# Performance work log

Hardware: AMD Instinct MI355X
Metric: run time of the kernel (lower is better)

The kernel has to match this reference:

```python
import jax, jax.numpy as jnp
import numpy as np

N = 50000
E = 800000
DIM = 64
MAX_DEG = 64
NUM_LAB = 16
BN_EPS = 1e-5
SLOPE = 0.01


def lrelu(x):
    return jnp.where(x > 0, x, SLOPE * x)


def batchnorm(x, w, b):
    m = x.mean(axis=0)
    v = x.var(axis=0)  # biased, matches torch BN normalization
    return (x - m) * jax.lax.rsqrt(v + BN_EPS) * w + b


def gin_conv(x, src, dst, wa, ba, wb, bb):
    # GINConv (eps=0): mlp(x + sum_{j->i} x_j); mlp = lin -> lrelu -> lin
    agg = jax.ops.segment_sum(x[src], dst, num_segments=x.shape[0])
    h = x + agg
    h = lrelu(h @ wa.T + ba)
    return h @ wb.T + bb


def setup_inputs() -> dict:
    key = jax.random.key(0)
    ks = iter(jax.random.split(key, 64))
    f = lambda *s: (jax.random.normal(next(ks), s, dtype=jnp.float32) * 0.1)
    dims = [2 * DIM, DIM, DIM, DIM]  # [128,64,64,64]
    inp = {
        'emb_deg': f(MAX_DEG, DIM),
        'emb_lab': f(NUM_LAB, DIM),
    }
    for i, (n1, n2) in enumerate(zip(dims[:-1], dims[1:])):
        inp[f'w{i}a'] = f(n1, n1)
        inp[f'b{i}a'] = f(n1)
        inp[f'w{i}b'] = f(n2, n1)
        inp[f'b{i}b'] = f(n2)
        inp[f'bn{i}_w'] = f(n2) + 1.0
        inp[f'bn{i}_b'] = f(n2)
    S = sum(dims)  # 320
    inp['fc1_w'] = f(DIM, S)
    inp['fc1_b'] = f(DIM)
    inp['fcbn_w'] = f(DIM) + 1.0
    inp['fcbn_b'] = f(DIM)
    inp['fc2_w'] = f(1, DIM)
    inp['fc2_b'] = f(1)
    inp['node_deg'] = jax.random.randint(next(ks), (N,), 0, MAX_DEG)
    inp['node_lab'] = jax.random.randint(next(ks), (N,), 0, NUM_LAB)
    inp['edge_index'] = jax.random.randint(next(ks), (2, E), 0, N)
    return inp


def reference(emb_deg, emb_lab,
              w0a, b0a, w0b, b0b, bn0_w, bn0_b,
              w1a, b1a, w1b, b1b, bn1_w, bn1_b,
              w2a, b2a, w2b, b2b, bn2_w, bn2_b,
              fc1_w, fc1_b, fcbn_w, fcbn_b, fc2_w, fc2_b,
              node_deg, node_lab, edge_index):
    src, dst = edge_index[0], edge_index[1]
    x0 = jnp.concatenate([emb_deg[node_deg], emb_lab[node_lab]], axis=1)  # [N, 2*DIM]
    z = [x0]
    layers = [(w0a, b0a, w0b, b0b, bn0_w, bn0_b),
              (w1a, b1a, w1b, b1b, bn1_w, bn1_b),
              (w2a, b2a, w2b, b2b, bn2_w, bn2_b)]
    for wa, ba, wb, bb, gw, gb in layers:
        x = gin_conv(z[-1], src, dst, wa, ba, wb, bb)
        x = lrelu(batchnorm(x, gw, gb))
        z.append(x)
    x = jnp.concatenate(z, axis=1)  # [N, sum(dims)]
    h = x @ fc1_w.T + fc1_b
    h = lrelu(batchnorm(h, fcbn_w, fcbn_b))
    out = jax.nn.sigmoid(h @ fc2_w.T + fc2_b)
    return out.squeeze(-1)  # [N]
```

## Files before the change

### kernel.cpp

```cpp
#include <hip/hip_runtime.h>

#define N_NODES 50000
#define E_EDGES 800000
#define BN_EPS 1e-5f
#define SLOPE 0.01f

#define SCAN_CHUNK 2048
#define SCAN_BLOCKS ((N_NODES + SCAN_CHUNK - 1) / SCAN_CHUNK)
#define STAT_SHARDS 32
#define FILL_PASSES 8

typedef unsigned short ushort_t;
typedef unsigned int uint_t;
typedef short short8 __attribute__((ext_vector_type(8)));
typedef float floatx4 __attribute__((ext_vector_type(4)));

__device__ __forceinline__ float ulo(uint_t v) { return __uint_as_float(v << 16); }
__device__ __forceinline__ float uhi(uint_t v) { return __uint_as_float(v & 0xffff0000u); }
__device__ __forceinline__ ushort_t f2b(float f) {
    uint_t u = __float_as_uint(f);
    return (ushort_t)((u + 0x7fffu + ((u >> 16) & 1u)) >> 16);
}
__device__ __forceinline__ uint_t pack2(float a, float b) {
    return (uint_t)f2b(a) | ((uint_t)f2b(b) << 16);
}

#define OWA0 0
#define OWB0 16384
#define OWA1 24576
#define OWB1 28672
#define OWA2 32768
#define OWB2 36864
#define OFC1 40960
#define WTOT 61440
#define CVT_BLOCKS ((WTOT + 255) / 256)
#define P_BLOCKS 48

__global__ void k_prep(const float* __restrict__ wa0, const float* __restrict__ wb0,
                       const float* __restrict__ wa1, const float* __restrict__ wb1,
                       const float* __restrict__ wa2, const float* __restrict__ wb2,
                       const float* __restrict__ fc1w, ushort_t* __restrict__ dst,
                       const float* __restrict__ ed, const float* __restrict__ el,
                       ushort_t* __restrict__ Pt) {
    int b = blockIdx.x, t = threadIdx.x;
    if (b < CVT_BLOCKS) {
        int i = b * 256 + t;
        if (i >= WTOT) return;
        float v;
        if      (i < OWB0) v = wa0[i];
        else if (i < OWA1) v = wb0[i - OWB0];
        else if (i < OWB1) v = wa1[i - OWA1];
        else if (i < OWA2) v = wb1[i - OWB1];
        else if (i < OWB2) v = wa2[i - OWA2];
        else if (i < OFC1) v = wb2[i - OWB2];
        else               v = fc1w[i - OFC1];
        dst[i] = f2b(v);
    } else {
        int pid = (b - CVT_BLOCKS) * 256 + t;
        int c = pid >> 7, j = pid & 127;
        float acc = 0.f;
        if (c < 64) {
            const float* dr = ed + c * 64;
            const float* wr = wa0 + (size_t)j * 128;
            #pragma unroll 8
            for (int k = 0; k < 64; ++k) acc += dr[k] * wr[k];
        } else if (c < 80) {
            const float* dr = el + (c - 64) * 64;
            const float* wr = wa0 + (size_t)j * 128 + 64;
            #pragma unroll 8
            for (int k = 0; k < 64; ++k) acc += dr[k] * wr[k];
        }
        Pt[(size_t)j * 96 + c] = f2b(acc);
    }
}

__global__ void k_build_x0(const float* __restrict__ ed, const float* __restrict__ el,
                           const int* __restrict__ nd, const int* __restrict__ nl,
                           uint_t* __restrict__ x0u, int* __restrict__ ncls) {
    int idx = blockIdx.x * blockDim.x + threadIdx.x;
    if (idx >= N_NODES * 64) return;
    int n = idx >> 6, c = idx & 63;
    int d = nd[n], l = nl[n];
    if (c == 0) ncls[n] = d | (l << 16);
    float2 v = (c < 32) ? *(const float2*)(ed + d * 64 + c * 2)
                        : *(const float2*)(el + l * 64 + (c - 32) * 2);
    x0u[(size_t)n * 64 + c] = pack2(v.x, v.y);
}

__global__ void k_degrank(const int* __restrict__ dst, int* __restrict__ deg,
                          int* __restrict__ rank) {
    int e = blockIdx.x * blockDim.x + threadIdx.x;
    if (e >= E_EDGES) return;
    rank[e] = atomicAdd(&deg[dst[e]], 1);
}

__global__ __launch_bounds__(256) void k_scan_a(const int* __restrict__ deg,
                                                int* __restrict__ bsum) {
    __shared__ int wsum[4];
    int t = threadIdx.x, b = blockIdx.x;
    int base = b * SCAN_CHUNK + t * 8;
    int s = 0;
    #pragma unroll
    for (int i = 0; i < 8; ++i) {
        int idx = base + i;
        if (idx < N_NODES) s += deg[idx];
    }
    #pragma unroll
    for (int o = 32; o; o >>= 1) s += __shfl_down(s, o);
    if ((t & 63) == 0) wsum[t >> 6] = s;
    __syncthreads();
    if (t == 0) bsum[b] = wsum[0] + wsum[1] + wsum[2] + wsum[3];
}

__global__ __launch_bounds__(256) void k_scan_c(const int* __restrict__ deg,
        const int* __restrict__ bsum, int* __restrict__ rowptr) {
    __shared__ int part[256];
    __shared__ int blockofs;
    int t = threadIdx.x, b = blockIdx.x;
    if (t < 64) {
        int v = (t < b) ? bsum[t] : 0;
        #pragma unroll
        for (int o = 32; o; o >>= 1) v += __shfl_down(v, o);
        if (t == 0) blockofs = v;
    }
    int base = b * SCAN_CHUNK + t * 8;
    int vals[8];
    int s = 0;
    #pragma unroll
    for (int i = 0; i < 8; ++i) {
        int idx = base + i;
        vals[i] = (idx < N_NODES) ? deg[idx] : 0;
        s += vals[i];
    }
    part[t] = s;
    __syncthreads();
    #pragma unroll
    for (int off = 1; off < 256; off <<= 1) {
        int v = (t >= off) ? part[t - off] : 0;
        __syncthreads();
        part[t] += v;
        __syncthreads();
    }
    int run = blockofs + part[t] - s;
    #pragma unroll
    for (int i = 0; i < 8; ++i) {
        int idx = base + i;
        if (idx < N_NODES) {
            rowptr[idx] = run;
            run += vals[i];
        }
    }
}

__global__ void k_fill(const int* __restrict__ src, const int* __restrict__ dst,
                       const int* __restrict__ ncls, const int* __restrict__ rowptr,
                       const int* __restrict__ rank, int* __restrict__ epk,
                       int blocks_per_pass) {
    int p = blockIdx.x / blocks_per_pass;
    int e = (blockIdx.x % blocks_per_pass) * blockDim.x + threadIdx.x;
    if (e >= E_EDGES) return;
    int d = dst[e];
    const int span = (N_NODES + FILL_PASSES - 1) / FILL_PASSES;
    int lo = p * span;
    if (d < lo || d >= lo + span) return;
    int s = src[e];
    int c = ncls[s];
    epk[rowptr[d] + rank[e]] = s | ((c & 63) << 16) | ((c >> 16) << 22);
}

__global__ __launch_bounds__(256, 8) void k_mlp0(
        const int* __restrict__ rowptr, const int* __restrict__ cdeg,
        const int* __restrict__ epk, const int* __restrict__ ncls,
        const ushort_t* __restrict__ Pt, const float* __restrict__ ba,
        const ushort_t* __restrict__ wbB, const float* __restrict__ bb,
        float* __restrict__ ybuf, float* __restrict__ stat_l) {
    constexpr int LHS = 98;
    constexpr int LDC = 104;
    constexpr int LDH = 136;
    __shared__ int hist[16 * LHS];
    __shared__ ushort_t xs[16 * LDC];
    __shared__ ushort_t hs[16 * LDH];
    uint_t* xsu = (uint_t*)xs;
    int t = threadIdx.x;
    int row0 = blockIdx.x * 16;
    int lane = t & 63, wv = t >> 6;
    int half = lane >> 5, hl = lane & 31;

    for (int i = t; i < 16 * LHS; i += 256) hist[i] = 0;
    __syncthreads();

    for (int i = 0; i < 2; ++i) {
        int lr = wv * 4 + i * 2 + half, node = row0 + lr;
        if (node < N_NODES) {
            if (hl == 0) {
                int c = ncls[node];
                atomicAdd(&hist[lr * LHS + (c & 0xffff)], 1);
                atomicAdd(&hist[lr * LHS + 64 + (c >> 16)], 1);
            }
            int start = rowptr[node], n = cdeg[node];
            for (int j0 = 0; j0 < n; j0 += 32) {
                int m = n - j0; if (m > 32) m = 32;
                if (hl < m) {
                    int ev = epk[start + j0 + hl];
                    atomicAdd(&hist[lr * LHS + ((ev >> 16) & 63)], 1);
                    atomicAdd(&hist[lr * LHS + 64 + ((ev >> 22) & 15)], 1);
                }
            }
        }
    }
    __syncthreads();

    for (int i = t; i < 16 * 48; i += 256) {
        int row = i / 48, c2 = i % 48;
        uint_t v = 0;
        if (c2 < 40)
            v = pack2((float)hist[row * LHS + c2 * 2],
                      (float)hist[row * LHS + c2 * 2 + 1]);
        xsu[row * 52 + c2] = v;
    }
    __syncthreads();

    int m = lane & 15, quad = lane >> 4;

    {
        floatx4 acc[2];
        acc[0] = (floatx4){0.f, 0.f, 0.f, 0.f};
        acc[1] = (floatx4){0.f, 0.f, 0.f, 0.f};
        #pragma unroll
        for (int ks = 0; ks < 3; ++ks) {
            short8 af = *(const short8*)(xs + m * LDC + ks * 32 + quad * 8);
            #pragma unroll
            for (int g = 0; g < 2; ++g) {
                int col = (wv * 2 + g) * 16 + m;
                short8 bf = *(const short8*)(Pt + (size_t)col * 96 + ks * 32 + quad * 8);
                acc[g] = __builtin_amdgcn_mfma_f32_16x16x32_bf16(af, bf, acc[g], 0, 0, 0);
            }
        }
        #pragma unroll
        for (int g = 0; g < 2; ++g) {
            int col = (wv * 2 + g) * 16 + m;
            float bias = ba[col];
            #pragma unroll
            for (int r = 0; r < 4; ++r) {
                float v = acc[g][r] + bias;
                v = v > 0.f ? v : SLOPE * v;
                hs[(quad * 4 + r) * LDH + col] = f2b(v);
            }
        }
    }
    __syncthreads();

    {
        floatx4 acc = (floatx4){0.f, 0.f, 0.f, 0.f};
        int col = wv * 16 + m;
        #pragma unroll
        for (int ks = 0; ks < 4; ++ks) {
            short8 af = *(const short8*)(hs + m * LDH + ks * 32 + quad * 8);
            short8 bf = *(const short8*)(wbB + (size_t)col * 128 + ks * 32 + quad * 8);
            acc = __builtin_amdgcn_mfma_f32_16x16x32_bf16(af, bf, acc, 0, 0, 0);
        }
        float bias = bb[col];
        float ps = 0.f, pq = 0.f;
        #pragma unroll
        for (int r = 0; r < 4; ++r) {
            int node = row0 + quad * 4 + r;
            float v = acc[r] + bias;
            if (node < N_NODES) ybuf[(size_t)node * 64 + col] = v;
            else v = 0.f;
            ps += v; pq += v * v;
        }
        ps += __shfl_xor(ps, 16); pq += __shfl_xor(pq, 16);
        ps += __shfl_xor(ps, 32); pq += __shfl_xor(pq, 32);
        if (quad == 0) {
            float* st = stat_l + (blockIdx.x & (STAT_SHARDS - 1)) * 128;
            atomicAdd(&st[col], ps);
            atomicAdd(&st[64 + col], pq);
        }
    }
}

__global__ __launch_bounds__(256, 8) void k_mlp64(
        const ushort_t* __restrict__ xb,
        const int* __restrict__ rowptr, const int* __restrict__ cdeg,
        const int* __restrict__ epk,
        const ushort_t* __restrict__ waB, const float* __restrict__ ba,
        const ushort_t* __restrict__ wbB, const float* __restrict__ bb,
        float* __restrict__ ybuf, float* __restrict__ stat_l) {
    constexpr int LDWB = 72;
    __shared__ ushort_t xs[16 * LDWB];
    __shared__ ushort_t hs[16 * LDWB];
    int t = threadIdx.x;
    int row0 = blockIdx.x * 16;
    int lane = t & 63, wv = t >> 6;
    int half = lane >> 5, hl = lane & 31;
    int g = hl >> 3, sseg = hl & 7;
    const uint4* xu4 = (const uint4*)xb;

    for (int i = 0; i < 2; ++i) {
        int lr = wv * 4 + i * 2 + half, node = row0 + lr;
        float acc[8] = {0.f, 0.f, 0.f, 0.f, 0.f, 0.f, 0.f, 0.f};
        if (node < N_NODES) {
            int start = rowptr[node], n = cdeg[node];
            if (g == 0) {
                uint4 v = xu4[(size_t)node * 8 + sseg];
                acc[0] += ulo(v.x); acc[1] += uhi(v.x);
                acc[2] += ulo(v.y); acc[3] += uhi(v.y);
                acc[4] += ulo(v.z); acc[5] += uhi(v.z);
                acc[6] += ulo(v.w); acc[7] += uhi(v.w);
            }
            for (int j0 = 0; j0 < n; j0 += 32) {
                int m = n - j0; if (m > 32) m = 32;
                int ev = (hl < m) ? epk[start + j0 + hl] : 0;
                int j = 0;
                for (; j + 8 <= m; j += 8) {
                    int sa = __shfl(ev, j + g, 32) & 0xffff;
                    int sb = __shfl(ev, j + 4 + g, 32) & 0xffff;
                    uint4 va = xu4[(size_t)sa * 8 + sseg];
                    uint4 vb = xu4[(size_t)sb * 8 + sseg];
                    acc[0] += ulo(va.x); acc[1] += uhi(va.x);
                    acc[2] += ulo(va.y); acc[3] += uhi(va.y);
                    acc[4] += ulo(va.z); acc[5] += uhi(va.z);
                    acc[6] += ulo(va.w); acc[7] += uhi(va.w);
                    acc[0] += ulo(vb.x); acc[1] += uhi(vb.x);
                    acc[2] += ulo(vb.y); acc[3] += uhi(vb.y);
                    acc[4] += ulo(vb.z); acc[5] += uhi(vb.z);
                    acc[6] += ulo(vb.w); acc[7] += uhi(vb.w);
                }
                for (; j < m; j += 4) {
                    int sa = __shfl(ev, j + g, 32) & 0xffff;
                    if (g < m - j) {
                        uint4 va = xu4[(size_t)sa * 8 + sseg];
                        acc[0] += ulo(va.x); acc[1] += uhi(va.x);
                        acc[2] += ulo(va.y); acc[3] += uhi(va.y);
                        acc[4] += ulo(va.z); acc[5] += uhi(va.z);
                        acc[6] += ulo(va.w); acc[7] += uhi(va.w);
                    }
                }
            }
        }
        #pragma unroll
        for (int q = 0; q < 8; ++q) {
            acc[q] += __shfl_xor(acc[q], 8, 32);
            acc[q] += __shfl_xor(acc[q], 16, 32);
        }
        if (g == 0) {
            uint4 pv = make_uint4(pack2(acc[0], acc[1]), pack2(acc[2], acc[3]),
                                  pack2(acc[4], acc[5]), pack2(acc[6], acc[7]));
            *(uint4*)(xs + lr * LDWB + sseg * 8) = pv;
        }
    }
    __syncthreads();

    int m = lane & 15, quad = lane >> 4;

    {
        floatx4 acc = (floatx4){0.f, 0.f, 0.f, 0.f};
        int col = wv * 16 + m;
        #pragma unroll
        for (int ks = 0; ks < 2; ++ks) {
            short8 af = *(const short8*)(xs + m * LDWB + ks * 32 + quad * 8);
            short8 bf = *(const short8*)(waB + (size_t)col * 64 + ks * 32 + quad * 8);
            acc = __builtin_amdgcn_mfma_f32_16x16x32_bf16(af, bf, acc, 0, 0, 0);
        }
        float bias = ba[col];
        #pragma unroll
        for (int r = 0; r < 4; ++r) {
            float v = acc[r] + bias;
            v = v > 0.f ? v : SLOPE * v;
            hs[(quad * 4 + r) * LDWB + col] = f2b(v);
        }
    }
    __syncthreads();

    {
        floatx4 acc = (floatx4){0.f, 0.f, 0.f, 0.f};
        int col = wv * 16 + m;
        #pragma unroll
        for (int ks = 0; ks < 2; ++ks) {
            short8 af = *(const short8*)(hs + m * LDWB + ks * 32 + quad * 8);
            short8 bf = *(const short8*)(wbB + (size_t)col * 64 + ks * 32 + quad * 8);
            acc = __builtin_amdgcn_mfma_f32_16x16x32_bf16(af, bf, acc, 0, 0, 0);
        }
        float bias = bb[col];
        float ps = 0.f, pq = 0.f;
        #pragma unroll
        for (int r = 0; r < 4; ++r) {
            int node = row0 + quad * 4 + r;
            float v = acc[r] + bias;
            if (node < N_NODES) ybuf[(size_t)node * 64 + col] = v;
            else v = 0.f;
            ps += v; pq += v * v;
        }
        ps += __shfl_xor(ps, 16); pq += __shfl_xor(pq, 16);
        ps += __shfl_xor(ps, 32); pq += __shfl_xor(pq, 32);
        if (quad == 0) {
            float* st = stat_l + (blockIdx.x & (STAT_SHARDS - 1)) * 128;
            atomicAdd(&st[col], ps);
            atomicAdd(&st[64 + col], pq);
        }
    }
}

__global__ void k_bn_apply(const float* __restrict__ y, const float* __restrict__ stat_l,
                           const float* __restrict__ gw, const float* __restrict__ gb,
                           uint_t* __restrict__ xo) {
    __shared__ float sc[64], sh[64];
    int t = threadIdx.x;
    if (t < 64) {
        float s0 = 0.f, q0 = 0.f;
        #pragma unroll
        for (int j = 0; j < STAT_SHARDS; ++j) {
            s0 += stat_l[j * 128 + t];
            q0 += stat_l[j * 128 + 64 + t];
        }
        float mmm = s0 * (1.0f / N_NODES);
        float var = q0 * (1.0f / N_NODES) - mmm * mmm;
        float s = gw[t] * rsqrtf(var + BN_EPS);
        sc[t] = s; sh[t] = gb[t] - mmm * s;
    }
    __syncthreads();
    int idx = blockIdx.x * blockDim.x + t;
    if (idx >= N_NODES * 16) return;
    int c4 = (idx & 15) * 4;
    float4 v4 = *(const float4*)(y + (size_t)idx * 4);
    float o0 = v4.x * sc[c4]     + sh[c4];     o0 = o0 > 0.f ? o0 : SLOPE * o0;
    float o1 = v4.y * sc[c4 + 1] + sh[c4 + 1]; o1 = o1 > 0.f ? o1 : SLOPE * o1;
    float o2 = v4.z * sc[c4 + 2] + sh[c4 + 2]; o2 = o2 > 0.f ? o2 : SLOPE * o2;
    float o3 = v4.w * sc[c4 + 3] + sh[c4 + 3]; o3 = o3 > 0.f ? o3 : SLOPE * o3;
    xo[(size_t)idx * 2]     = pack2(o0, o1);
    xo[(size_t)idx * 2 + 1] = pack2(o2, o3);
}

__global__ __launch_bounds__(256, 8) void k_fc1(
        const uint_t* __restrict__ x0u, const uint_t* __restrict__ x1u,
        const uint_t* __restrict__ x2u, const uint_t* __restrict__ x3u,
        const ushort_t* __restrict__ wB, const float* __restrict__ b,
        float* __restrict__ ybuf, float* __restrict__ stat_l) {
    constexpr int LDWB = 328;
    __shared__ ushort_t xs[16 * LDWB];
    uint_t* xsu = (uint_t*)xs;
    int t = threadIdx.x;
    int row0 = blockIdx.x * 16;

    for (int i = t; i < 16 * 160; i += 256) {
        int row = i / 160, c = i % 160;
        int g = row0 + row;
        uint_t v = 0;
        if (g < N_NODES) {
            if      (c < 64)  v = x0u[(size_t)g * 64 + c];
            else if (c < 96)  v = x1u[(size_t)g * 32 + (c - 64)];
            else if (c < 128) v = x2u[(size_t)g * 32 + (c - 96)];
            else              v = x3u[(size_t)g * 32 + (c - 128)];
        }
        xsu[row * 164 + c] = v;
    }
    __syncthreads();

    int lane = t & 63, wv = t >> 6;
    int m = lane & 15, quad = lane >> 4;
    int col = wv * 16 + m;
    floatx4 acc = (floatx4){0.f, 0.f, 0.f, 0.f};
    #pragma unroll
    for (int ks = 0; ks < 10; ++ks) {
        short8 af = *(const short8*)(xs + m * LDWB + ks * 32 + quad * 8);
        short8 bf = *(const short8*)(wB + (size_t)col * 320 + ks * 32 + quad * 8);
        acc = __builtin_amdgcn_mfma_f32_16x16x32_bf16(af, bf, acc, 0, 0, 0);
    }
    float bias = b[col];
    float ps = 0.f, pq = 0.f;
    #pragma unroll
    for (int r = 0; r < 4; ++r) {
        int node = row0 + quad * 4 + r;
        float v = acc[r] + bias;
        if (node < N_NODES) ybuf[(size_t)node * 64 + col] = v;
        else v = 0.f;
        ps += v; pq += v * v;
    }
    ps += __shfl_xor(ps, 16); pq += __shfl_xor(pq, 16);
    ps += __shfl_xor(ps, 32); pq += __shfl_xor(pq, 32);
    if (quad == 0) {
        float* st = stat_l + (blockIdx.x & (STAT_SHARDS - 1)) * 128;
        atomicAdd(&st[col], ps);
        atomicAdd(&st[64 + col], pq);
    }
}

__global__ void k_final(const float* __restrict__ y, const float* __restrict__ stat_l,
                        const float* __restrict__ gw, const float* __restrict__ gb,
                        const float* __restrict__ w2, const float* __restrict__ b2,
                        float* __restrict__ out) {
    __shared__ float sc[64], sh[64], w[64];
    int t = threadIdx.x;
    if (t < 64) {
        float s0 = 0.f, q0 = 0.f;
        #pragma unroll
        for (int j = 0; j < STAT_SHARDS; ++j) {
            s0 += stat_l[j * 128 + t];
            q0 += stat_l[j * 128 + 64 + t];
        }
        float mmm = s0 * (1.0f / N_NODES);
        float var = q0 * (1.0f / N_NODES) - mmm * mmm;
        float s = gw[t] * rsqrtf(var + BN_EPS);
        sc[t] = s; sh[t] = gb[t] - mmm * s; w[t] = w2[t];
    }
    __syncthreads();
    int i = blockIdx.x * blockDim.x + t;
    if (i >= N_NODES) return;
    float z = b2[0];
    const float* row = y + (size_t)i * 64;
    #pragma unroll
    for (int c = 0; c < 64; c += 4) {
        float4 v4 = *(const float4*)(row + c);
        float v;
        v = v4.x * sc[c]   + sh[c];   v = v > 0.f ? v : SLOPE * v; z += v * w[c];
        v = v4.y * sc[c+1] + sh[c+1]; v = v > 0.f ? v : SLOPE * v; z += v * w[c+1];
        v = v4.z * sc[c+2] + sh[c+2]; v = v > 0.f ? v : SLOPE * v; z += v * w[c+2];
        v = v4.w * sc[c+3] + sh[c+3]; v = v > 0.f ? v : SLOPE * v; z += v * w[c+3];
    }
    out[i] = 1.f / (1.f + __expf(-z));
}

extern "C" void kernel_launch(void* const* d_in, const int* in_sizes, int n_in,
                              void* d_out, int out_size, void* d_ws, size_t ws_size,
                              hipStream_t stream) {
    const float* emb_deg = (const float*)d_in[0];
    const float* emb_lab = (const float*)d_in[1];
    const float* wA[3]  = {(const float*)d_in[2],  (const float*)d_in[8],  (const float*)d_in[14]};
    const float* bA[3]  = {(const float*)d_in[3],  (const float*)d_in[9],  (const float*)d_in[15]};
    const float* wB[3]  = {(const float*)d_in[4],  (const float*)d_in[10], (const float*)d_in[16]};
    const float* bB[3]  = {(const float*)d_in[5],  (const float*)d_in[11], (const float*)d_in[17]};
    const float* bnw[3] = {(const float*)d_in[6],  (const float*)d_in[12], (const float*)d_in[18]};
    const float* bnb[3] = {(const float*)d_in[7],  (const float*)d_in[13], (const float*)d_in[19]};
    const float* fc1_w  = (const float*)d_in[20];
    const float* fc1_b  = (const float*)d_in[21];
    const float* fcbn_w = (const float*)d_in[22];
    const float* fcbn_b = (const float*)d_in[23];
    const float* fc2_w  = (const float*)d_in[24];
    const float* fc2_b  = (const float*)d_in[25];
    const int* node_deg = (const int*)d_in[26];
    const int* node_lab = (const int*)d_in[27];
    const int* src = (const int*)d_in[28];
    const int* dst = src + E_EDGES;
    float* out = (float*)d_out;

    float* ws   = (float*)d_ws;
    float* ybf  = ws;
    float* stat = ybf + (size_t)N_NODES * 64;
    uint_t* x0u = (uint_t*)(stat + 4 * STAT_SHARDS * 128);
    uint_t* x1u = x0u + (size_t)N_NODES * 64;
    uint_t* x2u = x1u + (size_t)N_NODES * 32;
    uint_t* x3u = x2u + (size_t)N_NODES * 32;
    int* epk    = (int*)(x3u + (size_t)N_NODES * 32);
    int* rank   = epk + E_EDGES;
    ushort_t* wbf = (ushort_t*)(rank + E_EDGES);
    ushort_t* Ptb = wbf + WTOT;
    int* cdeg   = (int*)(Ptb + 128 * 96);
    int* rowptr = cdeg + N_NODES;
    int* ncls   = rowptr + N_NODES;
    int* bsum   = ncls + N_NODES;

    const int RB = (N_NODES + 15) / 16;
    const int VB = (N_NODES * 16 + 255) / 256;
    const int HB = (N_NODES * 64 + 255) / 256;
    const int EB = (E_EDGES + 255) / 256;
    const int NB = (N_NODES + 255) / 256;

    hipMemsetAsync(stat, 0, (size_t)(4 * STAT_SHARDS * 128) * sizeof(float), stream);
    hipMemsetAsync(cdeg, 0, (size_t)N_NODES * sizeof(int), stream);

    k_prep<<<CVT_BLOCKS + P_BLOCKS, 256, 0, stream>>>(wA[0], wB[0], wA[1], wB[1],
        wA[2], wB[2], fc1_w, wbf, emb_deg, emb_lab, Ptb);
    k_build_x0<<<HB, 256, 0, stream>>>(emb_deg, emb_lab, node_deg, node_lab, x0u, ncls);

    k_degrank<<<EB, 256, 0, stream>>>(dst, cdeg, rank);
    k_scan_a<<<SCAN_BLOCKS, 256, 0, stream>>>(cdeg, bsum);
    k_scan_c<<<SCAN_BLOCKS, 256, 0, stream>>>(cdeg, bsum, rowptr);
    k_fill<<<FILL_PASSES * EB, 256, 0, stream>>>(src, dst, ncls, rowptr, rank, epk, EB);

    k_mlp0<<<RB, 256, 0, stream>>>(rowptr, cdeg, epk, ncls, Ptb, bA[0],
                                   wbf + OWB0, bB[0], ybf, stat);
    k_bn_apply<<<VB, 256, 0, stream>>>(ybf, stat, bnw[0], bnb[0], x1u);

    uint_t* xin[4] = {x0u, x1u, x2u, x3u};
    const ushort_t* waOfs[3] = {wbf + OWA0, wbf + OWA1, wbf + OWA2};
    const ushort_t* wbOfs[3] = {wbf + OWB0, wbf + OWB1, wbf + OWB2};
    for (int l = 1; l < 3; ++l) {
        float* st = stat + l * STAT_SHARDS * 128;
        k_mlp64<<<RB, 256, 0, stream>>>((const ushort_t*)xin[l], rowptr, cdeg, epk,
            waOfs[l], bA[l], wbOfs[l], bB[l], ybf, st);
        k_bn_apply<<<VB, 256, 0, stream>>>(ybf, st, bnw[l], bnb[l], xin[l + 1]);
    }

    float* stf = stat + 3 * STAT_SHARDS * 128;
    k_fc1<<<RB, 256, 0, stream>>>(x0u, x1u, x2u, x3u, wbf + OFC1, fc1_b, ybf, stf);
    k_final<<<NB, 256, 0, stream>>>(ybf, stf, fcbn_w, fcbn_b, fc2_w, fc2_b, out);
}
```

Measured before the change: 319.5 us.

## Merge front-end kernels, single-pass scan, fuse last BN-apply into fc1

Weight conversion, the embedding-table projection, x0 build, degree/rank atomics and the stat zeroing now run as one launch instead of four kernels plus a memset. The two-kernel block scan becomes one kernel in which each block redundantly sums all preceding degrees. The final layer's BN+LeakyReLU is applied inside fc1 as it loads its tile, which removes one bn_apply pass and the x3 buffer. The aim is fewer launches and less global traffic; the costs are extra prefix-sum reads in the scan and a stray negative-index read of wa2 that is then overwritten.

```diff
diff --git a/kernel.cpp b/kernel.cpp
--- a/kernel.cpp
+++ b/kernel.cpp
@@ -35,13 +35,20 @@
 #define WTOT 61440
 #define CVT_BLOCKS ((WTOT + 255) / 256)
 #define P_BLOCKS 48
-
-__global__ void k_prep(const float* __restrict__ wa0, const float* __restrict__ wb0,
-                       const float* __restrict__ wa1, const float* __restrict__ wb1,
-                       const float* __restrict__ wa2, const float* __restrict__ wb2,
-                       const float* __restrict__ fc1w, ushort_t* __restrict__ dst,
-                       const float* __restrict__ ed, const float* __restrict__ el,
-                       ushort_t* __restrict__ Pt) {
+#define X0_BLOCKS ((N_NODES * 64 + 255) / 256)
+#define E_BLOCKS ((E_EDGES + 255) / 256)
+#define STATZ_BLOCKS 16
+
+__global__ void k_front(const float* __restrict__ wa0, const float* __restrict__ wb0,
+                        const float* __restrict__ wa1, const float* __restrict__ wb1,
+                        const float* __restrict__ wa2, const float* __restrict__ wb2,
+                        const float* __restrict__ fc1w, ushort_t* __restrict__ wdst,
+                        const float* __restrict__ ed, const float* __restrict__ el,
+                        ushort_t* __restrict__ Pt,
+                        const int* __restrict__ nd, const int* __restrict__ nl,
+                        uint_t* __restrict__ x0u, int* __restrict__ ncls,
+                        const int* __restrict__ dst, int* __restrict__ deg,
+                        int* __restrict__ rank, float* __restrict__ stat) {
     int b = blockIdx.x, t = threadIdx.x;
     if (b < CVT_BLOCKS) {
         int i = b * 256 + t;
@@ -51,11 +58,12 @@
         else if (i < OWA1) v = wb0[i - OWB0];
         else if (i < OWB1) v = wa1[i - OWA1];
         else if (i < OWA2) v = wb1[i - OWB1];
-        else if (i < OWB2) v = wa2[i - OWA2];
+        else if (i < OWB2) v = wa2[i - OWB2 + OWA2 - OWA2];
         else if (i < OFC1) v = wb2[i - OWB2];
         else               v = fc1w[i - OFC1];
-        dst[i] = f2b(v);
-    } else {
+        if (i >= OWA2 && i < OWB2) v = wa2[i - OWA2];
+        wdst[i] = f2b(v);
+    } else if (b < CVT_BLOCKS + P_BLOCKS) {
         int pid = (b - CVT_BLOCKS) * 256 + t;
         int c = pid >> 7, j = pid & 127;
         float acc = 0.f;
@@ -71,58 +79,45 @@
             for (int k = 0; k < 64; ++k) acc += dr[k] * wr[k];
         }
         Pt[(size_t)j * 96 + c] = f2b(acc);
-    }
-}
-
-__global__ void k_build_x0(const float* __restrict__ ed, const float* __restrict__ el,
-                           const int* __restrict__ nd, const int* __restrict__ nl,
-                           uint_t* __restrict__ x0u, int* __restrict__ ncls) {
-    int idx = blockIdx.x * blockDim.x + threadIdx.x;
-    if (idx >= N_NODES * 64) return;
-    int n = idx >> 6, c = idx & 63;
-    int d = nd[n], l = nl[n];
-    if (c == 0) ncls[n] = d | (l << 16);
-    float2 v = (c < 32) ? *(const float2*)(ed + d * 64 + c * 2)
-                        : *(const float2*)(el + l * 64 + (c - 32) * 2);
-    x0u[(size_t)n * 64 + c] = pack2(v.x, v.y);
-}
-
-__global__ void k_degrank(const int* __restrict__ dst, int* __restrict__ deg,
-                          int* __restrict__ rank) {
-    int e = blockIdx.x * blockDim.x + threadIdx.x;
-    if (e >= E_EDGES) return;
-    rank[e] = atomicAdd(&deg[dst[e]], 1);
-}
-
-__global__ __launch_bounds__(256) void k_scan_a(const int* __restrict__ deg,
-                                                int* __restrict__ bsum) {
-    __shared__ int wsum[4];
+    } else if (b < CVT_BLOCKS + P_BLOCKS + X0_BLOCKS) {
+        int idx = (b - CVT_BLOCKS - P_BLOCKS) * 256 + t;
+        if (idx >= N_NODES * 64) return;
+        int n = idx >> 6, c = idx & 63;
+        int d = nd[n], l = nl[n];
+        if (c == 0) ncls[n] = d | (l << 16);
+        float2 v = (c < 32) ? *(const float2*)(ed + d * 64 + c * 2)
+                            : *(const float2*)(el + l * 64 + (c - 32) * 2);
+        x0u[(size_t)n * 64 + c] = pack2(v.x, v.y);
+    } else if (b < CVT_BLOCKS + P_BLOCKS + X0_BLOCKS + E_BLOCKS) {
+        int e = (b - CVT_BLOCKS - P_BLOCKS - X0_BLOCKS) * 256 + t;
+        if (e >= E_EDGES) return;
+        rank[e] = atomicAdd(&deg[dst[e]], 1);
+    } else {
+        int idx = (b - CVT_BLOCKS - P_BLOCKS - X0_BLOCKS - E_BLOCKS) * 256 + t;
+        if (idx < 4096)
+            *(float4*)(stat + (size_t)idx * 4) = make_float4(0.f, 0.f, 0.f, 0.f);
+    }
+}
+
+__global__ __launch_bounds__(256) void k_scan(const int* __restrict__ deg,
+                                              int* __restrict__ rowptr) {
+    __shared__ int part[256];
+    __shared__ int bofs_sh;
     int t = threadIdx.x, b = blockIdx.x;
-    int base = b * SCAN_CHUNK + t * 8;
-    int s = 0;
+    int pre = 0;
+    int lim = b * SCAN_CHUNK;
+    for (int i = t; i < lim; i += 256) pre += deg[i];
+    part[t] = pre;
+    __syncthreads();
     #pragma unroll
-    for (int i = 0; i < 8; ++i) {
-        int idx = base + i;
-        if (idx < N_NODES) s += deg[idx];
-    }
-    #pragma unroll
-    for (int o = 32; o; o >>= 1) s += __shfl_down(s, o);
-    if ((t & 63) == 0) wsum[t >> 6] = s;
-    __syncthreads();
-    if (t == 0) bsum[b] = wsum[0] + wsum[1] + wsum[2] + wsum[3];
-}
-
-__global__ __launch_bounds__(256) void k_scan_c(const int* __restrict__ deg,
-        const int* __restrict__ bsum, int* __restrict__ rowptr) {
-    __shared__ int part[256];
-    __shared__ int blockofs;
-    int t = threadIdx.x, b = blockIdx.x;
-    if (t < 64) {
-        int v = (t < b) ? bsum[t] : 0;
-        #pragma unroll
-        for (int o = 32; o; o >>= 1) v += __shfl_down(v, o);
-        if (t == 0) blockofs = v;
-    }
+    for (int off = 128; off; off >>= 1) {
+        if (t < off) part[t] += part[t + off];
+        __syncthreads();
+    }
+    if (t == 0) bofs_sh = part[0];
+    __syncthreads();
+    int bofs = bofs_sh;
+    __syncthreads();
     int base = b * SCAN_CHUNK + t * 8;
     int vals[8];
     int s = 0;
@@ -141,7 +136,7 @@
         part[t] += v;
         __syncthreads();
     }
-    int run = blockofs + part[t] - s;
+    int run = bofs + part[t] - s;
     #pragma unroll
     for (int i = 0; i < 8; ++i) {
         int idx = base + i;
@@ -433,14 +428,31 @@
 
 __global__ __launch_bounds__(256, 8) void k_fc1(
         const uint_t* __restrict__ x0u, const uint_t* __restrict__ x1u,
-        const uint_t* __restrict__ x2u, const uint_t* __restrict__ x3u,
+        const uint_t* __restrict__ x2u, const float* __restrict__ ybuf_in,
+        const float* __restrict__ stat2,
+        const float* __restrict__ gw2, const float* __restrict__ gb2,
         const ushort_t* __restrict__ wB, const float* __restrict__ b,
         float* __restrict__ ybuf, float* __restrict__ stat_l) {
     constexpr int LDWB = 328;
     __shared__ ushort_t xs[16 * LDWB];
+    __shared__ float sc2[64], sh2[64];
     uint_t* xsu = (uint_t*)xs;
     int t = threadIdx.x;
     int row0 = blockIdx.x * 16;
+
+    if (t < 64) {
+        float s0 = 0.f, q0 = 0.f;
+        #pragma unroll
+        for (int j = 0; j < STAT_SHARDS; ++j) {
+            s0 += stat2[j * 128 + t];
+            q0 += stat2[j * 128 + 64 + t];
+        }
+        float mmm = s0 * (1.0f / N_NODES);
+        float var = q0 * (1.0f / N_NODES) - mmm * mmm;
+        float s = gw2[t] * rsqrtf(var + BN_EPS);
+        sc2[t] = s; sh2[t] = gb2[t] - mmm * s;
+    }
+    __syncthreads();
 
     for (int i = t; i < 16 * 160; i += 256) {
         int row = i / 160, c = i % 160;
@@ -450,7 +462,15 @@
             if      (c < 64)  v = x0u[(size_t)g * 64 + c];
             else if (c < 96)  v = x1u[(size_t)g * 32 + (c - 64)];
             else if (c < 128) v = x2u[(size_t)g * 32 + (c - 96)];
-            else              v = x3u[(size_t)g * 32 + (c - 128)];
+            else {
+                int cc = (c - 128) * 2;
+                float2 yv = *(const float2*)(ybuf_in + (size_t)g * 64 + cc);
+                float o0 = yv.x * sc2[cc]     + sh2[cc];
+                float o1 = yv.y * sc2[cc + 1] + sh2[cc + 1];
+                o0 = o0 > 0.f ? o0 : SLOPE * o0;
+                o1 = o1 > 0.f ? o1 : SLOPE * o1;
+                v = pack2(o0, o1);
+            }
         }
         xsu[row * 164 + c] = v;
     }
@@ -549,49 +569,43 @@
     uint_t* x0u = (uint_t*)(stat + 4 * STAT_SHARDS * 128);
     uint_t* x1u = x0u + (size_t)N_NODES * 64;
     uint_t* x2u = x1u + (size_t)N_NODES * 32;
-    uint_t* x3u = x2u + (size_t)N_NODES * 32;
-    int* epk    = (int*)(x3u + (size_t)N_NODES * 32);
+    int* epk    = (int*)(x2u + (size_t)N_NODES * 32);
     int* rank   = epk + E_EDGES;
     ushort_t* wbf = (ushort_t*)(rank + E_EDGES);
     ushort_t* Ptb = wbf + WTOT;
     int* cdeg   = (int*)(Ptb + 128 * 96);
     int* rowptr = cdeg + N_NODES;
     int* ncls   = rowptr + N_NODES;
-    int* bsum   = ncls + N_NODES;
 
     const int RB = (N_NODES + 15) / 16;
     const int VB = (N_NODES * 16 + 255) / 256;
-    const int HB = (N_NODES * 64 + 255) / 256;
-    const int EB = (E_EDGES + 255) / 256;
     const int NB = (N_NODES + 255) / 256;
-
-    hipMemsetAsync(stat, 0, (size_t)(4 * STAT_SHARDS * 128) * sizeof(float), stream);
+    const int FRONT = CVT_BLOCKS + P_BLOCKS + X0_BLOCKS + E_BLOCKS + STATZ_BLOCKS;
+
     hipMemsetAsync(cdeg, 0, (size_t)N_NODES * sizeof(int), stream);
 
-    k_prep<<<CVT_BLOCKS + P_BLOCKS, 256, 0, stream>>>(wA[0], wB[0], wA[1], wB[1],
-        wA[2], wB[2], fc1_w, wbf, emb_deg, emb_lab, Ptb);
-    k_build_x0<<<HB, 256, 0, stream>>>(emb_deg, emb_lab, node_deg, node_lab, x0u, ncls);
-
-    k_degrank<<<EB, 256, 0, stream>>>(dst, cdeg, rank);
-    k_scan_a<<<SCAN_BLOCKS, 256, 0, stream>>>(cdeg, bsum);
-    k_scan_c<<<SCAN_BLOCKS, 256, 0, stream>>>(cdeg, bsum, rowptr);
-    k_fill<<<FILL_PASSES * EB, 256, 0, stream>>>(src, dst, ncls, rowptr, rank, epk, EB);
+    k_front<<<FRONT, 256, 0, stream>>>(wA[0], wB[0], wA[1], wB[1], wA[2], wB[2],
+        fc1_w, wbf, emb_deg, emb_lab, Ptb, node_deg, node_lab, x0u, ncls,
+        dst, cdeg, rank, stat);
+
+    k_scan<<<SCAN_BLOCKS, 256, 0, stream>>>(cdeg, rowptr);
+    k_fill<<<FILL_PASSES * E_BLOCKS, 256, 0, stream>>>(src, dst, ncls, rowptr,
+                                                       rank, epk, E_BLOCKS);
 
     k_mlp0<<<RB, 256, 0, stream>>>(rowptr, cdeg, epk, ncls, Ptb, bA[0],
                                    wbf + OWB0, bB[0], ybf, stat);
     k_bn_apply<<<VB, 256, 0, stream>>>(ybf, stat, bnw[0], bnb[0], x1u);
 
-    uint_t* xin[4] = {x0u, x1u, x2u, x3u};
-    const ushort_t* waOfs[3] = {wbf + OWA0, wbf + OWA1, wbf + OWA2};
-    const ushort_t* wbOfs[3] = {wbf + OWB0, wbf + OWB1, wbf + OWB2};
-    for (int l = 1; l < 3; ++l) {
-        float* st = stat + l * STAT_SHARDS * 128;
-        k_mlp64<<<RB, 256, 0, stream>>>((const ushort_t*)xin[l], rowptr, cdeg, epk,
-            waOfs[l], bA[l], wbOfs[l], bB[l], ybf, st);
-        k_bn_apply<<<VB, 256, 0, stream>>>(ybf, st, bnw[l], bnb[l], xin[l + 1]);
-    }
+    k_mlp64<<<RB, 256, 0, stream>>>((const ushort_t*)x1u, rowptr, cdeg, epk,
+        wbf + OWA1, bA[1], wbf + OWB1, bB[1], ybf, stat + STAT_SHARDS * 128);
+    k_bn_apply<<<VB, 256, 0, stream>>>(ybf, stat + STAT_SHARDS * 128,
+                                       bnw[1], bnb[1], x2u);
+
+    k_mlp64<<<RB, 256, 0, stream>>>((const ushort_t*)x2u, rowptr, cdeg, epk,
+        wbf + OWA2, bA[2], wbf + OWB2, bB[2], ybf, stat + 2 * STAT_SHARDS * 128);
 
     float* stf = stat + 3 * STAT_SHARDS * 128;
-    k_fc1<<<RB, 256, 0, stream>>>(x0u, x1u, x2u, x3u, wbf + OFC1, fc1_b, ybf, stf);
+    k_fc1<<<RB, 256, 0, stream>>>(x0u, x1u, x2u, ybf, stat + 2 * STAT_SHARDS * 128,
+        bnw[2], bnb[2], wbf + OFC1, fc1_b, ybf, stf);
     k_final<<<NB, 256, 0, stream>>>(ybf, stf, fcbn_w, fcbn_b, fc2_w, fc2_b, out);
 }
```

After: 345.1 us. 8.0% more time.
